# Optimization experiments

Hardware: AMD Instinct MI355X
Metric: run time of the kernel (lower is better)

The kernel has to match this reference:

```python
import jax, jax.numpy as jnp
import numpy as np

TEMPERATURE = 0.05
EPS = 1e-8  # torch.cosine_similarity eps


def setup_inputs() -> dict:
    key = jax.random.key(0)
    k1, k2 = jax.random.split(key)
    N, D = 8192, 256
    text_embeddings = jax.random.normal(k1, (N, D), dtype=jnp.float32)
    text_pos_embeddings = jax.random.normal(k2, (N, D), dtype=jnp.float32)
    return {"text_embeddings": text_embeddings, "text_pos_embeddings": text_pos_embeddings}


def reference(text_embeddings, text_pos_embeddings):
    # cosine similarity via normalize + single GEMM (same math as broadcasted
    # torch.cosine_similarity, which clamps norms at eps)
    a_norm = jnp.maximum(jnp.linalg.norm(text_embeddings, axis=-1, keepdims=True), EPS)
    b_norm = jnp.maximum(jnp.linalg.norm(text_pos_embeddings, axis=-1, keepdims=True), EPS)
    a = text_embeddings / a_norm  # [N, D]
    b = text_pos_embeddings / b_norm  # [N, D]
    sim = jnp.einsum("nd,md->nm", a, b) / TEMPERATURE  # [N, N]
    # cross-entropy with labels = arange(N): mean over rows of -log_softmax diag
    logp = jax.nn.log_softmax(sim, axis=-1)
    loss = -jnp.mean(jnp.diagonal(logp))
    return loss
```

## Files before the change

kernel.cpp:

```cpp
#include <hip/hip_runtime.h>
#include <hip/hip_bf16.h>
#include <math.h>

#define DIM 256

typedef __bf16 bf16x8 __attribute__((ext_vector_type(8)));
typedef float f32x4 __attribute__((ext_vector_type(4)));

__constant__ const float kTempInvLog2e = 20.0f * 1.4426950408889634f;
#define LN2 0.6931471805599453f
#define EPS_NORM 1e-8f

static __device__ inline unsigned short f2bf(float f) {
    unsigned u = __builtin_bit_cast(unsigned, f);
    unsigned r = (u + 0x7fffu + ((u >> 16) & 1u)) >> 16;
    return (unsigned short)r;
}
static __device__ inline unsigned pack2(float x, float y, float s) {
    return (unsigned)f2bf(x * s) | ((unsigned)f2bf(y * s) << 16);
}

__global__ __launch_bounds__(256) void normpack_kernel(
    const float* __restrict__ A, const float* __restrict__ B,
    unsigned short* __restrict__ Apk, unsigned short* __restrict__ Bpk,
    float* __restrict__ diag, int n)
{
    __shared__ uint4 lA[512];
    __shared__ uint4 lB[512];
    const int t = threadIdx.x;
    const int rl = t >> 4;
    const int c16 = t & 15;
    const int r = blockIdx.x * 16 + rl;

    const float4* pa = (const float4*)(A + (size_t)r * DIM + c16 * 16);
    const float4* pb = (const float4*)(B + (size_t)r * DIM + c16 * 16);
    float4 a0 = pa[0], a1 = pa[1], a2 = pa[2], a3 = pa[3];
    float4 b0 = pb[0], b1 = pb[1], b2 = pb[2], b3 = pb[3];

    float ssa = a0.x*a0.x + a0.y*a0.y + a0.z*a0.z + a0.w*a0.w
              + a1.x*a1.x + a1.y*a1.y + a1.z*a1.z + a1.w*a1.w
              + a2.x*a2.x + a2.y*a2.y + a2.z*a2.z + a2.w*a2.w
              + a3.x*a3.x + a3.y*a3.y + a3.z*a3.z + a3.w*a3.w;
    float ssb = b0.x*b0.x + b0.y*b0.y + b0.z*b0.z + b0.w*b0.w
              + b1.x*b1.x + b1.y*b1.y + b1.z*b1.z + b1.w*b1.w
              + b2.x*b2.x + b2.y*b2.y + b2.z*b2.z + b2.w*b2.w
              + b3.x*b3.x + b3.y*b3.y + b3.z*b3.z + b3.w*b3.w;
    float dd  = a0.x*b0.x + a0.y*b0.y + a0.z*b0.z + a0.w*b0.w
              + a1.x*b1.x + a1.y*b1.y + a1.z*b1.z + a1.w*b1.w
              + a2.x*b2.x + a2.y*b2.y + a2.z*b2.z + a2.w*b2.w
              + a3.x*b3.x + a3.y*b3.y + a3.z*b3.z + a3.w*b3.w;
#pragma unroll
    for (int m = 1; m < 16; m <<= 1) {
        ssa += __shfl_xor(ssa, m, 64);
        ssb += __shfl_xor(ssb, m, 64);
        dd  += __shfl_xor(dd, m, 64);
    }
    float na = fmaxf(sqrtf(ssa), EPS_NORM);
    float nb = fmaxf(sqrtf(ssb), EPS_NORM);
    float sa = kTempInvLog2e / na;
    float sb = 1.0f / nb;
    if (c16 == 0) diag[r] = dd / (na * nb) * kTempInvLog2e;

    const int k0 = c16 >> 1;
    const int q0 = (c16 & 1) * 2;
    const int p0 = k0 * 64 + rl + q0 * 16;
    uint4 ga0, ga1, gb0, gb1;
    ga0.x = pack2(a0.x, a0.y, sa); ga0.y = pack2(a0.z, a0.w, sa);
    ga0.z = pack2(a1.x, a1.y, sa); ga0.w = pack2(a1.z, a1.w, sa);
    ga1.x = pack2(a2.x, a2.y, sa); ga1.y = pack2(a2.z, a2.w, sa);
    ga1.z = pack2(a3.x, a3.y, sa); ga1.w = pack2(a3.z, a3.w, sa);
    gb0.x = pack2(b0.x, b0.y, sb); gb0.y = pack2(b0.z, b0.w, sb);
    gb0.z = pack2(b1.x, b1.y, sb); gb0.w = pack2(b1.z, b1.w, sb);
    gb1.x = pack2(b2.x, b2.y, sb); gb1.y = pack2(b2.z, b2.w, sb);
    gb1.z = pack2(b3.x, b3.y, sb); gb1.w = pack2(b3.z, b3.w, sb);
    lA[p0] = ga0; lA[p0 + 16] = ga1;
    lB[p0] = gb0; lB[p0 + 16] = gb1;
    __syncthreads();

    const size_t gbase = (size_t)blockIdx.x * 512 + 2 * t;
    ((uint4*)Apk)[gbase]     = lA[2 * t];
    ((uint4*)Apk)[gbase + 1] = lA[2 * t + 1];
    ((uint4*)Bpk)[gbase]     = lB[2 * t];
    ((uint4*)Bpk)[gbase + 1] = lB[2 * t + 1];
}

#define LOAD_BT(buf, bt)                                                     \
    {                                                                        \
        const bf16x8* _p = (const bf16x8*)(Bpk + ((size_t)(bt) * 512 + lane) * 8); \
        _Pragma("unroll")                                                    \
        for (int k = 0; k < 8; ++k)                                          \
            buf[k] = _p[k * 8];                                              \
    }

#define COMPUTE_TILE(buf)                                                    \
    {                                                                        \
        f32x4 acc[4];                                                        \
        _Pragma("unroll")                                                    \
        for (int m = 0; m < 4; ++m) acc[m] = (f32x4){0.f, 0.f, 0.f, 0.f};    \
        _Pragma("unroll")                                                    \
        for (int k = 0; k < 8; ++k) {                                        \
            _Pragma("unroll")                                                \
            for (int m = 0; m < 4; ++m)                                      \
                acc[m] = __builtin_amdgcn_mfma_f32_16x16x32_bf16(            \
                    afrag[m][k], buf[k], acc[m], 0, 0, 0);                   \
        }                                                                    \
        _Pragma("unroll")                                                    \
        for (int m = 0; m < 4; ++m)                                          \
            _Pragma("unroll")                                                \
            for (int r = 0; r < 4; ++r)                                      \
                sums[m * 4 + r] += __builtin_amdgcn_exp2f(acc[m][r]);        \
    }

__global__ __launch_bounds__(64, 2) void gemm_lse_kernel(
    const unsigned short* __restrict__ Apk, const unsigned short* __restrict__ Bpk,
    float* __restrict__ partial, int n)
{
    const int lane = threadIdx.x;
    const int c = lane & 15;
    const int q = lane >> 4;

    const int i = blockIdx.x;
    const int split = ((i & 7) << 1) | ((i >> 3) & 1);
    const int rowblk = i >> 4;
    const int rowbase = rowblk * 64;

    bf16x8 afrag[4][8];
    const int atile0 = rowblk * 4;
#pragma unroll
    for (int m = 0; m < 4; ++m)
#pragma unroll
        for (int k = 0; k < 8; ++k)
            afrag[m][k] = *(const bf16x8*)(Apk + ((size_t)(atile0 + m) * 512 + k * 64 + lane) * 8);
#pragma unroll
    for (int m = 0; m < 4; ++m)
#pragma unroll
        for (int k = 0; k < 8; ++k)
            asm volatile("" : "+v"(*(f32x4*)&afrag[m][k]));

    float sums[16];
#pragma unroll
    for (int s = 0; s < 16; ++s) sums[s] = 0.0f;

    const int btile0 = split * 32;
    bf16x8 b0[8], b1[8];
    LOAD_BT(b0, btile0);

    for (int it = 0; it < 32; it += 2) {
        LOAD_BT(b1, btile0 + it + 1);
        COMPUTE_TILE(b0);
        LOAD_BT(b0, btile0 + it + 2);
        COMPUTE_TILE(b1);
    }

#pragma unroll
    for (int s = 0; s < 16; ++s) {
        float v = sums[s];
        v += __shfl_xor(v, 1, 64);
        v += __shfl_xor(v, 2, 64);
        v += __shfl_xor(v, 4, 64);
        v += __shfl_xor(v, 8, 64);
        sums[s] = v;
    }
    if (c == 0) {
#pragma unroll
        for (int m = 0; m < 4; ++m)
#pragma unroll
            for (int r = 0; r < 4; ++r)
                partial[(size_t)(rowbase + m * 16 + q * 4 + r) * 16 + split] = sums[m * 4 + r];
    }
}

__global__ __launch_bounds__(256) void row_lse_kernel(
    const float* __restrict__ partial, const float* __restrict__ diag,
    float* __restrict__ bsum, int n)
{
    __shared__ float red[256];
    const int row = blockIdx.x * 256 + threadIdx.x;
    float local = 0.0f;
    if (row < n) {
        const float4* p = (const float4*)(partial + (size_t)row * 16);
        float4 p0 = p[0], p1 = p[1], p2 = p[2], p3 = p[3];
        float s = (p0.x + p0.y + p0.z + p0.w) + (p1.x + p1.y + p1.z + p1.w)
                + (p2.x + p2.y + p2.z + p2.w) + (p3.x + p3.y + p3.z + p3.w);
        local = log2f(s) - diag[row];
    }
    red[threadIdx.x] = local;
    __syncthreads();
    for (int off = 128; off > 0; off >>= 1) {
        if (threadIdx.x < off) red[threadIdx.x] += red[threadIdx.x + off];
        __syncthreads();
    }
    if (threadIdx.x == 0) bsum[blockIdx.x] = red[0];
}

__global__ __launch_bounds__(64) void final_kernel(
    const float* __restrict__ bsum, float* __restrict__ out, int nblocks, int n)
{
    float v = (threadIdx.x < nblocks) ? bsum[threadIdx.x] : 0.0f;
#pragma unroll
    for (int m = 1; m < 64; m <<= 1) v += __shfl_xor(v, m, 64);
    if (threadIdx.x == 0) out[0] = v * (LN2 / (float)n);
}

extern "C" void kernel_launch(void* const* d_in, const int* in_sizes, int n_in,
                              void* d_out, int out_size, void* d_ws, size_t ws_size,
                              hipStream_t stream) {
    const int n = in_sizes[0] / DIM;
    const float* A = (const float*)d_in[0];
    const float* B = (const float*)d_in[1];
    float* out = (float*)d_out;

    unsigned short* Apk = (unsigned short*)d_ws;
    unsigned short* Bpk = Apk + (size_t)n * DIM;
    float* partial = (float*)(Bpk + (size_t)n * DIM);
    float* diag = partial + (size_t)n * 16;
    float* bsum = diag + n;

    normpack_kernel<<<n / 16, 256, 0, stream>>>(A, B, Apk, Bpk, diag, n);

    gemm_lse_kernel<<<(n / 64) * 16, 64, 0, stream>>>(Apk, Bpk, partial, n);

    const int nred = (n + 255) / 256;
    row_lse_kernel<<<nred, 256, 0, stream>>>(partial, diag, bsum, n);
    final_kernel<<<1, 64, 0, stream>>>(bsum, out, nred, n);
}
```

Before: 110.2 us.

## Switch similarity GEMM from bf16 to fp8 e4m3 MFMA with finer column split

```diff
diff --git a/kernel.cpp b/kernel.cpp
--- a/kernel.cpp
+++ b/kernel.cpp
@@ -1,32 +1,28 @@
 #include <hip/hip_runtime.h>
 #include <hip/hip_bf16.h>
+#include <hip/hip_fp8.h>
 #include <math.h>
 
 #define DIM 256
 
-typedef __bf16 bf16x8 __attribute__((ext_vector_type(8)));
 typedef float f32x4 __attribute__((ext_vector_type(4)));
 
 __constant__ const float kTempInvLog2e = 20.0f * 1.4426950408889634f;
 #define LN2 0.6931471805599453f
 #define EPS_NORM 1e-8f
 
-static __device__ inline unsigned short f2bf(float f) {
-    unsigned u = __builtin_bit_cast(unsigned, f);
-    unsigned r = (u + 0x7fffu + ((u >> 16) & 1u)) >> 16;
-    return (unsigned short)r;
-}
-static __device__ inline unsigned pack2(float x, float y, float s) {
-    return (unsigned)f2bf(x * s) | ((unsigned)f2bf(y * s) << 16);
+static __device__ inline unsigned f2fp8x4(float4 v, float s) {
+    __hip_fp8_e4m3 a(v.x * s), b(v.y * s), c(v.z * s), d(v.w * s);
+    return (unsigned)a.__x | ((unsigned)b.__x << 8) | ((unsigned)c.__x << 16) | ((unsigned)d.__x << 24);
 }
 
 __global__ __launch_bounds__(256) void normpack_kernel(
     const float* __restrict__ A, const float* __restrict__ B,
-    unsigned short* __restrict__ Apk, unsigned short* __restrict__ Bpk,
+    unsigned char* __restrict__ Apk, unsigned char* __restrict__ Bpk,
     float* __restrict__ diag, int n)
 {
-    __shared__ uint4 lA[512];
-    __shared__ uint4 lB[512];
+    __shared__ uint2 lA[512];
+    __shared__ uint2 lB[512];
     const int t = threadIdx.x;
     const int rl = t >> 4;
     const int c16 = t & 15;
@@ -64,32 +60,29 @@
     const int k0 = c16 >> 1;
     const int q0 = (c16 & 1) * 2;
     const int p0 = k0 * 64 + rl + q0 * 16;
-    uint4 ga0, ga1, gb0, gb1;
-    ga0.x = pack2(a0.x, a0.y, sa); ga0.y = pack2(a0.z, a0.w, sa);
-    ga0.z = pack2(a1.x, a1.y, sa); ga0.w = pack2(a1.z, a1.w, sa);
-    ga1.x = pack2(a2.x, a2.y, sa); ga1.y = pack2(a2.z, a2.w, sa);
-    ga1.z = pack2(a3.x, a3.y, sa); ga1.w = pack2(a3.z, a3.w, sa);
-    gb0.x = pack2(b0.x, b0.y, sb); gb0.y = pack2(b0.z, b0.w, sb);
-    gb0.z = pack2(b1.x, b1.y, sb); gb0.w = pack2(b1.z, b1.w, sb);
-    gb1.x = pack2(b2.x, b2.y, sb); gb1.y = pack2(b2.z, b2.w, sb);
-    gb1.z = pack2(b3.x, b3.y, sb); gb1.w = pack2(b3.z, b3.w, sb);
+    uint2 ga0, ga1, gb0, gb1;
+    ga0.x = f2fp8x4(a0, sa); ga0.y = f2fp8x4(a1, sa);
+    ga1.x = f2fp8x4(a2, sa); ga1.y = f2fp8x4(a3, sa);
+    gb0.x = f2fp8x4(b0, sb); gb0.y = f2fp8x4(b1, sb);
+    gb1.x = f2fp8x4(b2, sb); gb1.y = f2fp8x4(b3, sb);
     lA[p0] = ga0; lA[p0 + 16] = ga1;
     lB[p0] = gb0; lB[p0 + 16] = gb1;
     __syncthreads();
 
-    const size_t gbase = (size_t)blockIdx.x * 512 + 2 * t;
-    ((uint4*)Apk)[gbase]     = lA[2 * t];
-    ((uint4*)Apk)[gbase + 1] = lA[2 * t + 1];
-    ((uint4*)Bpk)[gbase]     = lB[2 * t];
-    ((uint4*)Bpk)[gbase + 1] = lB[2 * t + 1];
+    uint2 xa0 = lA[2 * t], xa1 = lA[2 * t + 1];
+    uint2 xb0 = lB[2 * t], xb1 = lB[2 * t + 1];
+    uint4 oa; oa.x = xa0.x; oa.y = xa0.y; oa.z = xa1.x; oa.w = xa1.y;
+    uint4 ob; ob.x = xb0.x; ob.y = xb0.y; ob.z = xb1.x; ob.w = xb1.y;
+    ((uint4*)Apk)[(size_t)blockIdx.x * 256 + t] = oa;
+    ((uint4*)Bpk)[(size_t)blockIdx.x * 256 + t] = ob;
 }
 
 #define LOAD_BT(buf, bt)                                                     \
     {                                                                        \
-        const bf16x8* _p = (const bf16x8*)(Bpk + ((size_t)(bt) * 512 + lane) * 8); \
+        const long* _p = (const long*)Bpk + (size_t)(bt) * 512 + lane;       \
         _Pragma("unroll")                                                    \
         for (int k = 0; k < 8; ++k)                                          \
-            buf[k] = _p[k * 8];                                              \
+            buf[k] = _p[k * 64];                                             \
     }
 
 #define COMPUTE_TILE(buf)                                                    \
@@ -101,7 +94,7 @@
         for (int k = 0; k < 8; ++k) {                                        \
             _Pragma("unroll")                                                \
             for (int m = 0; m < 4; ++m)                                      \
-                acc[m] = __builtin_amdgcn_mfma_f32_16x16x32_bf16(            \
+                acc[m] = __builtin_amdgcn_mfma_f32_16x16x32_fp8_fp8(         \
                     afrag[m][k], buf[k], acc[m], 0, 0, 0);                   \
         }                                                                    \
         _Pragma("unroll")                                                    \
@@ -111,8 +104,8 @@
                 sums[m * 4 + r] += __builtin_amdgcn_exp2f(acc[m][r]);        \
     }
 
-__global__ __launch_bounds__(64, 2) void gemm_lse_kernel(
-    const unsigned short* __restrict__ Apk, const unsigned short* __restrict__ Bpk,
+__global__ __launch_bounds__(64, 3) void gemm_lse_kernel(
+    const unsigned char* __restrict__ Apk, const unsigned char* __restrict__ Bpk,
     float* __restrict__ partial, int n)
 {
     const int lane = threadIdx.x;
@@ -120,32 +113,34 @@
     const int q = lane >> 4;
 
     const int i = blockIdx.x;
-    const int split = ((i & 7) << 1) | ((i >> 3) & 1);
-    const int rowblk = i >> 4;
+    const int split = ((i & 7) << 2) | ((i >> 3) & 3);
+    const int rowblk = i >> 5;
     const int rowbase = rowblk * 64;
 
-    bf16x8 afrag[4][8];
+    long afrag[4][8];
     const int atile0 = rowblk * 4;
 #pragma unroll
+    for (int m = 0; m < 4; ++m) {
+        const long* ap = (const long*)Apk + (size_t)(atile0 + m) * 512 + lane;
+#pragma unroll
+        for (int k = 0; k < 8; ++k)
+            afrag[m][k] = ap[k * 64];
+    }
+#pragma unroll
     for (int m = 0; m < 4; ++m)
 #pragma unroll
         for (int k = 0; k < 8; ++k)
-            afrag[m][k] = *(const bf16x8*)(Apk + ((size_t)(atile0 + m) * 512 + k * 64 + lane) * 8);
-#pragma unroll
-    for (int m = 0; m < 4; ++m)
-#pragma unroll
-        for (int k = 0; k < 8; ++k)
-            asm volatile("" : "+v"(*(f32x4*)&afrag[m][k]));
+            asm volatile("" : "+v"(afrag[m][k]));
 
     float sums[16];
 #pragma unroll
     for (int s = 0; s < 16; ++s) sums[s] = 0.0f;
 
-    const int btile0 = split * 32;
-    bf16x8 b0[8], b1[8];
+    const int btile0 = split * 16;
+    long b0[8], b1[8];
     LOAD_BT(b0, btile0);
 
-    for (int it = 0; it < 32; it += 2) {
+    for (int it = 0; it < 16; it += 2) {
         LOAD_BT(b1, btile0 + it + 1);
         COMPUTE_TILE(b0);
         LOAD_BT(b0, btile0 + it + 2);
@@ -166,7 +161,7 @@
         for (int m = 0; m < 4; ++m)
 #pragma unroll
             for (int r = 0; r < 4; ++r)
-                partial[(size_t)(rowbase + m * 16 + q * 4 + r) * 16 + split] = sums[m * 4 + r];
+                partial[(size_t)(rowbase + m * 16 + q * 4 + r) * 32 + split] = sums[m * 4 + r];
     }
 }
 
@@ -178,10 +173,13 @@
     const int row = blockIdx.x * 256 + threadIdx.x;
     float local = 0.0f;
     if (row < n) {
-        const float4* p = (const float4*)(partial + (size_t)row * 16);
-        float4 p0 = p[0], p1 = p[1], p2 = p[2], p3 = p[3];
-        float s = (p0.x + p0.y + p0.z + p0.w) + (p1.x + p1.y + p1.z + p1.w)
-                + (p2.x + p2.y + p2.z + p2.w) + (p3.x + p3.y + p3.z + p3.w);
+        const float4* p = (const float4*)(partial + (size_t)row * 32);
+        float s = 0.0f;
+#pragma unroll
+        for (int j = 0; j < 8; ++j) {
+            float4 v = p[j];
+            s += (v.x + v.y) + (v.z + v.w);
+        }
         local = log2f(s) - diag[row];
     }
     red[threadIdx.x] = local;
@@ -210,15 +208,15 @@
     const float* B = (const float*)d_in[1];
     float* out = (float*)d_out;
 
-    unsigned short* Apk = (unsigned short*)d_ws;
-    unsigned short* Bpk = Apk + (size_t)n * DIM;
+    unsigned char* Apk = (unsigned char*)d_ws;
+    unsigned char* Bpk = Apk + (size_t)n * DIM;
     float* partial = (float*)(Bpk + (size_t)n * DIM);
-    float* diag = partial + (size_t)n * 16;
+    float* diag = partial + (size_t)n * 32;
     float* bsum = diag + n;
 
     normpack_kernel<<<n / 16, 256, 0, stream>>>(A, B, Apk, Bpk, diag, n);
 
-    gemm_lse_kernel<<<(n / 64) * 16, 64, 0, stream>>>(Apk, Bpk, partial, n);
+    gemm_lse_kernel<<<(n / 64) * 32, 64, 0, stream>>>(Apk, Bpk, partial, n);
 
     const int nred = (n + 255) / 256;
     row_lse_kernel<<<nred, 256, 0, stream>>>(partial, diag, bsum, n);
```

Result: no change. 110.0 us (-0.2%).
